# Performance work log

Hardware: AMD Instinct MI355X
Metric: run time of the kernel (lower is better)

Reference implementation:

```python
import jax, jax.numpy as jnp
import numpy as np

CUTOFF = 5.0
NLINKED = 1
CELL_LIST = CUTOFF / NLINKED  # linked-cell edge length
_r = np.arange(-NLINKED, NLINKED + 1)
# torch.cartesian_prod(r1,r1,r1) == meshgrid(indexing='ij') stacked & flattened
LINKED = np.stack(np.meshgrid(_r, _r, _r, indexing='ij'), axis=-1).reshape(1, -1, 3).astype(np.float32)  # (1, 27, 3)


def setup_inputs() -> dict:
    N = 2744
    L = 30.0
    key = jax.random.key(0)
    k1, k2 = jax.random.split(key)
    coordinates = jax.random.uniform(k1, (N, 3), dtype=jnp.float32) * L
    cell = jnp.eye(3, dtype=jnp.float32) * L
    mass = jax.random.uniform(k2, (N,), dtype=jnp.float32) * 15.0 + 1.0
    period_table = jnp.ones((3,), dtype=jnp.int32)  # fully periodic
    return {"period_table": period_table, "coordinates": coordinates, "cell": cell, "mass": mass}


def _forward(period_table, coordinates, cell, mass):
    numatom = coordinates.shape[0]
    # wrap coordinates into the cell relative to atom 0 (fractional coords)
    inv_cell = jnp.linalg.inv(cell)
    inv_coor = coordinates @ inv_cell
    inv_coor = inv_coor - jnp.round(inv_coor - inv_coor[0])
    coordinates = inv_coor @ cell
    # remove center of mass
    com = (mass @ coordinates) / jnp.sum(mass)
    coordinates = coordinates - com[None, :]
    # periodic replicas needed to cover the cutoff
    num_repeats = jnp.ceil(jnp.min(CUTOFF / jnp.abs(cell), axis=0)).astype(jnp.int32)
    num_repeats = period_table.astype(jnp.int32) * num_repeats
    up = num_repeats + 1
    down = -num_repeats
    rs = [jnp.arange(int(down[i]), int(up[i])) for i in range(3)]
    g = jnp.meshgrid(*rs, indexing='ij')
    shifts_frac = jnp.stack(g, axis=-1).reshape(-1, 3).astype(coordinates.dtype)  # (S, 3)
    shifts = shifts_frac @ cell  # (S, 3) cartesian shift vectors
    num_shifts = shifts.shape[0]
    # prod = cartesian_prod(all_shifts, all_atoms).T : row0 shift idx, row1 atom idx
    prod0 = jnp.repeat(jnp.arange(num_shifts), numatom)
    prod1 = jnp.tile(jnp.arange(numatom), num_shifts)
    # shift box so all coords are positive; pad by cutoff
    mincoor = jnp.min(coordinates, axis=0) - CUTOFF - 1e-6
    coordinates = coordinates - mincoor
    maxcoor = jnp.max(coordinates, axis=0) + CUTOFF
    # all periodic images, keep only those inside the padded box
    image = (coordinates[None, :, :] + shifts[:, None, :]).reshape(-1, 3)
    keep = jnp.nonzero(((image < maxcoor) & (image > 0)).all(axis=1))[0]
    image_mask = image[keep]                      # (M, 3)
    prod0 = prod0[keep]
    prod1 = prod1[keep]
    # linked-cell indices
    ori_image_index = jnp.floor(coordinates / CELL_LIST)         # (N, 3)
    neigh_cell = ori_image_index[:, None, :] + jnp.asarray(LINKED)  # (N, 27, 3)
    image_index = jnp.floor(image_mask / CELL_LIST)              # (M, 3)
    max_cell_index = jnp.ceil(maxcoor / CELL_LIST)
    f10 = max_cell_index[1] * max_cell_index[0]
    neigh_cell_index = neigh_cell[:, :, 2] * f10 + neigh_cell[:, :, 1] * max_cell_index[0] + neigh_cell[:, :, 0]  # (N, 27)
    nimage_index = image_index[:, 2] * f10 + image_index[:, 1] * max_cell_index[0] + image_index[:, 0]            # (M,)
    # dense (N, M, 27) cell-index equality -- the memory-bound hot spot
    eq = neigh_cell_index[:, None, :] == nimage_index[None, :, None]
    ai, aj, _ = jnp.nonzero(eq)
    # distance filter on candidate pairs
    d = jnp.linalg.norm(coordinates[ai] - image_mask[aj], axis=-1)
    pair = jnp.nonzero((d < CUTOFF) & (d > 0.001))[0]
    center = ai[pair]
    img = aj[pair]
    shift_idx = prod0[img]
    atom_j = prod1[img]
    neigh_list = jnp.stack([center, atom_j])  # (2, P)
    return neigh_list, shifts[shift_idx], shifts_frac, shift_idx


def reference(period_table, coordinates, cell, mass):
    neigh_list, shifts_out, _, _ = _forward(period_table, coordinates, cell, mass)
    return (neigh_list, shifts_out)
```

## Files before the change

kernel.cpp:

```cpp
#include <hip/hip_runtime.h>
#include <math.h>

#define S_CAP   27
#define NCELLS  4096
#define MAXNB   128
#define CUT     5.0f

__global__ __launch_bounds__(256)
void k1_pre(const int* __restrict__ period, const float* __restrict__ coor,
            const float* __restrict__ cell, const float* __restrict__ mass,
            int* hdr_i, float* hdr_f, float* shifts, float* xf,
            int* __restrict__ ccount, int* __restrict__ ccur, int n)
{
    #pragma clang fp contract(off)
    __shared__ double rs[256 * 4];
    __shared__ float  redf[256 * 3];
    __shared__ float  s_com[3], s_m2[3];
    int t = threadIdx.x;

    for (int c = t; c < NCELLS; c += 256) { ccount[c] = 0; ccur[c] = 0; }

    float c[3][3];
    #pragma unroll
    for (int i = 0; i < 3; i++)
        #pragma unroll
        for (int j = 0; j < 3; j++) c[i][j] = cell[3 * i + j];

    float a00 = c[1][1]*c[2][2] - c[1][2]*c[2][1];
    float a01 = c[0][2]*c[2][1] - c[0][1]*c[2][2];
    float a02 = c[0][1]*c[1][2] - c[0][2]*c[1][1];
    float a10 = c[1][2]*c[2][0] - c[1][0]*c[2][2];
    float a11 = c[0][0]*c[2][2] - c[0][2]*c[2][0];
    float a12 = c[0][2]*c[1][0] - c[0][0]*c[1][2];
    float a20 = c[1][0]*c[2][1] - c[1][1]*c[2][0];
    float a21 = c[0][1]*c[2][0] - c[0][0]*c[2][1];
    float a22 = c[0][0]*c[1][1] - c[0][1]*c[1][0];
    float det = c[0][0]*a00 + c[0][1]*a10 + c[0][2]*a20;
    float inv[3][3] = {{a00/det, a01/det, a02/det},
                       {a10/det, a11/det, a12/det},
                       {a20/det, a21/det, a22/det}};

    float f0[3];
    #pragma unroll
    for (int d = 0; d < 3; d++)
        f0[d] = coor[0]*inv[0][d] + coor[1]*inv[1][d] + coor[2]*inv[2][d];

    double sm = 0.0, sx = 0.0, sy = 0.0, sz = 0.0;
    for (int i = t; i < n; i += 256) {
        float p0 = coor[3*i], p1 = coor[3*i+1], p2 = coor[3*i+2];
        float ic[3], w[3], x[3];
        #pragma unroll
        for (int d = 0; d < 3; d++)
            ic[d] = p0*inv[0][d] + p1*inv[1][d] + p2*inv[2][d];
        #pragma unroll
        for (int d = 0; d < 3; d++)
            w[d] = ic[d] - rintf(ic[d] - f0[d]);
        #pragma unroll
        for (int d = 0; d < 3; d++)
            x[d] = w[0]*c[0][d] + w[1]*c[1][d] + w[2]*c[2][d];
        xf[3*i] = x[0]; xf[3*i+1] = x[1]; xf[3*i+2] = x[2];
        float m = mass[i];
        sm += (double)m;
        sx += (double)m * (double)x[0];
        sy += (double)m * (double)x[1];
        sz += (double)m * (double)x[2];
    }
    rs[t] = sm; rs[256+t] = sx; rs[512+t] = sy; rs[768+t] = sz;
    __syncthreads();
    for (int off = 128; off > 0; off >>= 1) {
        if (t < off) {
            rs[t]       += rs[t+off];
            rs[256+t]   += rs[256+t+off];
            rs[512+t]   += rs[512+t+off];
            rs[768+t]   += rs[768+t+off];
        }
        __syncthreads();
    }
    if (t == 0) {
        float den = (float)rs[0];
        s_com[0] = ((float)rs[256]) / den;
        s_com[1] = ((float)rs[512]) / den;
        s_com[2] = ((float)rs[768]) / den;
    }
    __syncthreads();
    float com0 = s_com[0], com1 = s_com[1], com2 = s_com[2];

    float mn0 = __builtin_inff(), mn1 = __builtin_inff(), mn2 = __builtin_inff();
    for (int i = t; i < n; i += 256) {
        float v0 = xf[3*i]   - com0;
        float v1 = xf[3*i+1] - com1;
        float v2 = xf[3*i+2] - com2;
        xf[3*i] = v0; xf[3*i+1] = v1; xf[3*i+2] = v2;
        mn0 = fminf(mn0, v0); mn1 = fminf(mn1, v1); mn2 = fminf(mn2, v2);
    }
    redf[t] = mn0; redf[256+t] = mn1; redf[512+t] = mn2;
    __syncthreads();
    for (int off = 128; off > 0; off >>= 1) {
        if (t < off) {
            redf[t]     = fminf(redf[t],     redf[t+off]);
            redf[256+t] = fminf(redf[256+t], redf[256+t+off]);
            redf[512+t] = fminf(redf[512+t], redf[512+t+off]);
        }
        __syncthreads();
    }
    if (t == 0) {
        s_m2[0] = (redf[0]   - CUT) - 1e-6f;
        s_m2[1] = (redf[256] - CUT) - 1e-6f;
        s_m2[2] = (redf[512] - CUT) - 1e-6f;
    }
    __syncthreads();
    float m20 = s_m2[0], m21 = s_m2[1], m22 = s_m2[2];

    float mx0 = -__builtin_inff(), mx1 = -__builtin_inff(), mx2 = -__builtin_inff();
    for (int i = t; i < n; i += 256) {
        float v0 = xf[3*i]   - m20;
        float v1 = xf[3*i+1] - m21;
        float v2 = xf[3*i+2] - m22;
        xf[3*i] = v0; xf[3*i+1] = v1; xf[3*i+2] = v2;
        mx0 = fmaxf(mx0, v0); mx1 = fmaxf(mx1, v1); mx2 = fmaxf(mx2, v2);
    }
    redf[t] = mx0; redf[256+t] = mx1; redf[512+t] = mx2;
    __syncthreads();
    for (int off = 128; off > 0; off >>= 1) {
        if (t < off) {
            redf[t]     = fmaxf(redf[t],     redf[t+off]);
            redf[256+t] = fmaxf(redf[256+t], redf[256+t+off]);
            redf[512+t] = fmaxf(redf[512+t], redf[512+t+off]);
        }
        __syncthreads();
    }
    if (t == 0) {
        float maxc0 = redf[0]   + CUT;
        float maxc1 = redf[256] + CUT;
        float maxc2 = redf[512] + CUT;
        float mcell0 = ceilf(maxc0 / CUT);
        float mcell1 = ceilf(maxc1 / CUT);
        float f10 = mcell1 * mcell0;
        int nr[3];
        for (int j = 0; j < 3; j++) {
            float v = __builtin_inff();
            for (int i = 0; i < 3; i++) {
                float q = CUT / fabsf(c[i][j]);
                v = fminf(v, q);
            }
            nr[j] = (int)ceilf(v);
            nr[j] *= period[j];
        }
        int nsz0 = 2*nr[0]+1, nsz1 = 2*nr[1]+1, nsz2 = 2*nr[2]+1;
        int S = nsz0 * nsz1 * nsz2;
        if (S > S_CAP) S = S_CAP;
        hdr_i[0] = S;
        hdr_i[3] = -nr[0]; hdr_i[4] = -nr[1]; hdr_i[5] = -nr[2];
        hdr_i[6] = nsz0;   hdr_i[7] = nsz1;   hdr_i[8] = nsz2;
        hdr_i[9]  = (int)mcell0;
        hdr_i[10] = (int)f10;
        hdr_f[0] = maxc0; hdr_f[1] = maxc1; hdr_f[2] = maxc2;
        hdr_f[3] = f10;   hdr_f[4] = mcell0;
    }
    __syncthreads();
    int S = hdr_i[0];
    if (t < S) {
        int n1 = hdr_i[7], n2 = hdr_i[8];
        int i0 = t / (n1 * n2);
        int rem = t - i0 * n1 * n2;
        int i1 = rem / n2;
        int i2 = rem - i1 * n2;
        float fx = (float)(hdr_i[3] + i0);
        float fy = (float)(hdr_i[4] + i1);
        float fz = (float)(hdr_i[5] + i2);
        #pragma unroll
        for (int d = 0; d < 3; d++)
            shifts[3*t + d] = fx*c[0][d] + fy*c[1][d] + fz*c[2][d];
    }
}

__global__ __launch_bounds__(256)
void k2_count(const int* __restrict__ hdr_i, const float* __restrict__ hdr_f,
              const float* __restrict__ shifts, const float* __restrict__ xf,
              int* __restrict__ ccount, int n)
{
    #pragma clang fp contract(off)
    int g = blockIdx.x * 256 + threadIdx.x;
    int sn = hdr_i[0] * n;
    if (g >= sn) return;
    int s = g / n, a = g - s * n;
    float i0 = xf[3*a]   + shifts[3*s];
    float i1 = xf[3*a+1] + shifts[3*s+1];
    float i2 = xf[3*a+2] + shifts[3*s+2];
    bool k = (i0 > 0.0f) && (i0 < hdr_f[0]) &&
             (i1 > 0.0f) && (i1 < hdr_f[1]) &&
             (i2 > 0.0f) && (i2 < hdr_f[2]);
    if (!k) return;
    float fc0 = floorf(i0 / CUT);
    float fc1 = floorf(i1 / CUT);
    float fc2 = floorf(i2 / CUT);
    float cf = fc2 * hdr_f[3] + fc1 * hdr_f[4] + fc0;
    int ci = (int)cf;
    if (ci < 0) ci = 0;
    if (ci >= NCELLS) ci = NCELLS - 1;
    atomicAdd(&ccount[ci], 1);
}

__global__ __launch_bounds__(1024)
void k5_scan(const int* __restrict__ ccount, int* __restrict__ cstart)
{
    __shared__ int sarr[1024];
    int t = threadIdx.x;
    int b = t * 4;
    int v0 = ccount[b], v1 = ccount[b+1], v2 = ccount[b+2], v3 = ccount[b+3];
    int lsum = v0 + v1 + v2 + v3;
    sarr[t] = lsum;
    __syncthreads();
    for (int off = 1; off < 1024; off <<= 1) {
        int v = (t >= off) ? sarr[t - off] : 0;
        __syncthreads();
        sarr[t] += v;
        __syncthreads();
    }
    int excl = sarr[t] - lsum;
    cstart[b]   = excl;
    cstart[b+1] = excl + v0;
    cstart[b+2] = excl + v0 + v1;
    cstart[b+3] = excl + v0 + v1 + v2;
    if (t == 1023) cstart[NCELLS] = sarr[1023];
}

__global__ __launch_bounds__(256)
void k5b_fill(const int* __restrict__ hdr_i, const float* __restrict__ hdr_f,
              const float* __restrict__ shifts, const float* __restrict__ xf,
              const int* __restrict__ cstart, int* __restrict__ ccur,
              float4* __restrict__ bucket4, int n)
{
    #pragma clang fp contract(off)
    int g = blockIdx.x * 256 + threadIdx.x;
    int sn = hdr_i[0] * n;
    if (g >= sn) return;
    int s = g / n, a = g - s * n;
    float i0 = xf[3*a]   + shifts[3*s];
    float i1 = xf[3*a+1] + shifts[3*s+1];
    float i2 = xf[3*a+2] + shifts[3*s+2];
    bool k = (i0 > 0.0f) && (i0 < hdr_f[0]) &&
             (i1 > 0.0f) && (i1 < hdr_f[1]) &&
             (i2 > 0.0f) && (i2 < hdr_f[2]);
    if (!k) return;
    float fc0 = floorf(i0 / CUT);
    float fc1 = floorf(i1 / CUT);
    float fc2 = floorf(i2 / CUT);
    float cf = fc2 * hdr_f[3] + fc1 * hdr_f[4] + fc0;
    int ci = (int)cf;
    if (ci < 0) ci = 0;
    if (ci >= NCELLS) ci = NCELLS - 1;
    int w = cstart[ci] + atomicAdd(&ccur[ci], 1);
    bucket4[w] = make_float4(i0, i1, i2, __int_as_float(g));
}

__global__ __launch_bounds__(256)
void k6_count(const int* __restrict__ hdr_i, const float* __restrict__ xf,
              const int* __restrict__ cstart, const float4* __restrict__ bucket4,
              int* __restrict__ npair, int n)
{
    #pragma clang fp contract(off)
    int lane = threadIdx.x & 63;
    int atom = (blockIdx.x * 256 + threadIdx.x) >> 6;
    if (atom >= n) return;
    int mci = hdr_i[9], f10i = hdr_i[10];
    float x0 = xf[3*atom], x1 = xf[3*atom+1], x2 = xf[3*atom+2];
    int o0 = (int)floorf(x0 / CUT);
    int o1 = (int)floorf(x1 / CUT);
    int o2 = (int)floorf(x2 / CUT);
    int cnt = 0;
    for (int dz = -1; dz <= 1; dz++)
        for (int dy = -1; dy <= 1; dy++) {
            int nc0 = (o2+dz)*f10i + (o1+dy)*mci + (o0-1);
            int lo = nc0 < 0 ? 0 : nc0;
            int hi = nc0 + 3 > NCELLS ? NCELLS : nc0 + 3;
            if (lo >= hi) continue;
            int b0 = cstart[lo], b1 = cstart[hi];
            for (int b = b0 + lane; b < b1; b += 64) {
                float4 v = bucket4[b];
                float dxx = x0 - v.x;
                float dyy = x1 - v.y;
                float dzz = x2 - v.z;
                float ss = dxx*dxx + dyy*dyy + dzz*dzz;
                float dd = sqrtf(ss);
                if (dd < CUT && dd > 0.001f) cnt++;
            }
        }
    #pragma unroll
    for (int off = 32; off > 0; off >>= 1)
        cnt += __shfl_down(cnt, off, 64);
    if (lane == 0) npair[atom] = cnt;
}

__global__ __launch_bounds__(1024)
void k7_scan(int* hdr_i, const int* __restrict__ npair, int* __restrict__ pstart, int n)
{
    __shared__ int sarr[1024];
    int t = threadIdx.x;
    int CH = (n + 1023) >> 10;
    int base = t * CH;
    int lsum = 0;
    for (int e = 0; e < CH; e++) {
        int g = base + e;
        if (g < n) lsum += npair[g];
    }
    sarr[t] = lsum;
    __syncthreads();
    for (int off = 1; off < 1024; off <<= 1) {
        int v = (t >= off) ? sarr[t - off] : 0;
        __syncthreads();
        sarr[t] += v;
        __syncthreads();
    }
    int run = sarr[t] - lsum;
    for (int e = 0; e < CH; e++) {
        int g = base + e;
        if (g < n) { pstart[g] = run; run += npair[g]; }
    }
    if (t == 1023) pstart[n] = sarr[1023];
    if (t == 0)    hdr_i[2]  = sarr[1023];
}

__global__ __launch_bounds__(256)
void k8_emit(const int* __restrict__ hdr_i, const float* __restrict__ xf,
             const float* __restrict__ shifts, const int* __restrict__ cstart,
             const float4* __restrict__ bucket4, const int* __restrict__ pstart,
             float* __restrict__ out, int n, int P)
{
    #pragma clang fp contract(off)
    __shared__ int lst[4][MAXNB];
    int w    = threadIdx.x >> 6;
    int lane = threadIdx.x & 63;
    int atom = blockIdx.x * 4 + w;
    bool valid = atom < n;

    int mci = hdr_i[9], f10i = hdr_i[10];
    float x0 = 0.f, x1 = 0.f, x2 = 0.f;
    if (valid) { x0 = xf[3*atom]; x1 = xf[3*atom+1]; x2 = xf[3*atom+2]; }
    int o0 = (int)floorf(x0 / CUT);
    int o1 = (int)floorf(x1 / CUT);
    int o2 = (int)floorf(x2 / CUT);

    int cnt = 0;
    if (valid) {
        for (int dz = -1; dz <= 1; dz++)
            for (int dy = -1; dy <= 1; dy++) {
                int nc0 = (o2+dz)*f10i + (o1+dy)*mci + (o0-1);
                int lo = nc0 < 0 ? 0 : nc0;
                int hi = nc0 + 3 > NCELLS ? NCELLS : nc0 + 3;
                if (lo >= hi) continue;
                int b0 = cstart[lo], b1 = cstart[hi];
                for (int bb = b0; bb < b1; bb += 64) {
                    int b = bb + lane;
                    bool ok = false; int g = 0;
                    if (b < b1) {
                        float4 v = bucket4[b];
                        g = __float_as_int(v.w);
                        float dxx = x0 - v.x;
                        float dyy = x1 - v.y;
                        float dzz = x2 - v.z;
                        float ss = dxx*dxx + dyy*dyy + dzz*dzz;
                        float dd = sqrtf(ss);
                        ok = (dd < CUT) && (dd > 0.001f);
                    }
                    unsigned long long m = __ballot(ok);
                    int posn = cnt + (int)__popcll(m & ((1ull << lane) - 1ull));
                    if (ok && posn < MAXNB) lst[w][posn] = g;
                    cnt += (int)__popcll(m);
                }
            }
        if (cnt > MAXNB) cnt = MAXNB;
    }
    __syncthreads();

    if (valid) {
        int base = pstart[atom];
        for (int r = lane; r < cnt; r += 64) {
            int g = lst[w][r];
            int rank = 0;
            for (int q = 0; q < cnt; q++) rank += (lst[w][q] < g) ? 1 : 0;
            int p = base + rank;
            if (p < P) {
                int s = g / n;
                int a = g - s * n;
                out[p]     = (float)atom;
                out[P + p] = (float)a;
                out[2*P + 3*p]     = shifts[3*s];
                out[2*P + 3*p + 1] = shifts[3*s + 1];
                out[2*P + 3*p + 2] = shifts[3*s + 2];
            }
        }
    }
}

extern "C" void kernel_launch(void* const* d_in, const int* in_sizes, int n_in,
                              void* d_out, int out_size, void* d_ws, size_t ws_size,
                              hipStream_t stream)
{
    const int*   period = (const int*)d_in[0];
    const float* coor   = (const float*)d_in[1];
    const float* cell   = (const float*)d_in[2];
    const float* mass   = (const float*)d_in[3];
    float* out = (float*)d_out;

    int n  = in_sizes[1] / 3;
    int SN = S_CAP * n;
    int P  = out_size / 5;

    char* w = (char*)d_ws;
    size_t off = 0;
    auto alloc = [&](size_t bytes) -> void* {
        off = (off + 15) & ~(size_t)15;
        void* p = (void*)(w + off); off += bytes; return p;
    };

    int*    hdr_i   = (int*)   alloc(16 * 4);
    float*  hdr_f   = (float*) alloc(16 * 4);
    float*  shifts  = (float*) alloc(3 * S_CAP * 4);
    float*  xf      = (float*) alloc(3 * (size_t)n * 4);
    int*    ccount  = (int*)   alloc(NCELLS * 4);
    int*    ccur    = (int*)   alloc(NCELLS * 4);
    int*    cstart  = (int*)   alloc((NCELLS + 1) * 4);
    float4* bucket4 = (float4*)alloc((size_t)SN * 16);
    int*    npair   = (int*)   alloc((size_t)n * 4);
    int*    pstart  = (int*)   alloc(((size_t)n + 1) * 4);
    (void)ws_size; (void)n_in;

    hipMemsetAsync(d_out, 0, (size_t)out_size * 4, stream);

    int nwb = (n + 3) / 4;

    hipLaunchKernelGGL(k1_pre,   dim3(1),            dim3(256),  0, stream,
                       period, coor, cell, mass, hdr_i, hdr_f, shifts, xf, ccount, ccur, n);
    hipLaunchKernelGGL(k2_count, dim3((SN+255)/256), dim3(256),  0, stream,
                       hdr_i, hdr_f, shifts, xf, ccount, n);
    hipLaunchKernelGGL(k5_scan,  dim3(1),            dim3(1024), 0, stream,
                       ccount, cstart);
    hipLaunchKernelGGL(k5b_fill, dim3((SN+255)/256), dim3(256),  0, stream,
                       hdr_i, hdr_f, shifts, xf, cstart, ccur, bucket4, n);
    hipLaunchKernelGGL(k6_count, dim3(nwb),          dim3(256),  0, stream,
                       hdr_i, xf, cstart, bucket4, npair, n);
    hipLaunchKernelGGL(k7_scan,  dim3(1),            dim3(1024), 0, stream,
                       hdr_i, npair, pstart, n);
    hipLaunchKernelGGL(k8_emit,  dim3(nwb),          dim3(256),  0, stream,
                       hdr_i, xf, shifts, cstart, bucket4, pstart, out, n, P);
}
```

Before: 108.7 us.

## Fuse scans into last-block epilogues and cache neighbor lists between count and emit

Replaces the two single-block scan kernels with last-block-done epilogues inside the count kernels, using a global atomic ticket. This cuts the launch chain from seven launches to five. The pair-count kernel now writes each atom's candidate neighbor list to a global slab, so the emit kernel reads it instead of redoing the cell search. The k1 min/max reductions are merged into one pass, with the min offset applied on the fly rather than via an extra rewrite pass. The output memset is dropped. The cost is that the reductions are serialized through one block's tail and per-atom slab memory traffic is added. Dropping the memset risks leaving stale output beyond the emitted pair count.

Result: slower. 159.4 us (+46.7%).

```diff
diff --git a/kernel.cpp b/kernel.cpp
--- a/kernel.cpp
+++ b/kernel.cpp
@@ -6,19 +6,21 @@
 #define MAXNB   128
 #define CUT     5.0f
 
+
 __global__ __launch_bounds__(256)
 void k1_pre(const int* __restrict__ period, const float* __restrict__ coor,
             const float* __restrict__ cell, const float* __restrict__ mass,
-            int* hdr_i, float* hdr_f, float* shifts, float* xf,
+            int* hdr_i, float* hdr_f, float* shifts, float* xv,
             int* __restrict__ ccount, int* __restrict__ ccur, int n)
 {
     #pragma clang fp contract(off)
     __shared__ double rs[256 * 4];
-    __shared__ float  redf[256 * 3];
+    __shared__ float  redf[256 * 6];
     __shared__ float  s_com[3], s_m2[3];
     int t = threadIdx.x;
 
     for (int c = t; c < NCELLS; c += 256) { ccount[c] = 0; ccur[c] = 0; }
+    if (t < 2) hdr_i[12 + t] = 0;
 
     float c[3][3];
     #pragma unroll
@@ -58,7 +60,7 @@
         #pragma unroll
         for (int d = 0; d < 3; d++)
             x[d] = w[0]*c[0][d] + w[1]*c[1][d] + w[2]*c[2][d];
-        xf[3*i] = x[0]; xf[3*i+1] = x[1]; xf[3*i+2] = x[2];
+        xv[3*i] = x[0]; xv[3*i+1] = x[1]; xv[3*i+2] = x[2];
         float m = mass[i];
         sm += (double)m;
         sx += (double)m * (double)x[0];
@@ -69,10 +71,10 @@
     __syncthreads();
     for (int off = 128; off > 0; off >>= 1) {
         if (t < off) {
-            rs[t]       += rs[t+off];
-            rs[256+t]   += rs[256+t+off];
-            rs[512+t]   += rs[512+t+off];
-            rs[768+t]   += rs[768+t+off];
+            rs[t]     += rs[t+off];
+            rs[256+t] += rs[256+t+off];
+            rs[512+t] += rs[512+t+off];
+            rs[768+t] += rs[768+t+off];
         }
         __syncthreads();
     }
@@ -85,54 +87,38 @@
     __syncthreads();
     float com0 = s_com[0], com1 = s_com[1], com2 = s_com[2];
 
-    float mn0 = __builtin_inff(), mn1 = __builtin_inff(), mn2 = __builtin_inff();
+    float mn0 =  __builtin_inff(), mn1 =  __builtin_inff(), mn2 =  __builtin_inff();
+    float mx0 = -__builtin_inff(), mx1 = -__builtin_inff(), mx2 = -__builtin_inff();
     for (int i = t; i < n; i += 256) {
-        float v0 = xf[3*i]   - com0;
-        float v1 = xf[3*i+1] - com1;
-        float v2 = xf[3*i+2] - com2;
-        xf[3*i] = v0; xf[3*i+1] = v1; xf[3*i+2] = v2;
+        float v0 = xv[3*i]   - com0;
+        float v1 = xv[3*i+1] - com1;
+        float v2 = xv[3*i+2] - com2;
+        xv[3*i] = v0; xv[3*i+1] = v1; xv[3*i+2] = v2;
         mn0 = fminf(mn0, v0); mn1 = fminf(mn1, v1); mn2 = fminf(mn2, v2);
-    }
-    redf[t] = mn0; redf[256+t] = mn1; redf[512+t] = mn2;
+        mx0 = fmaxf(mx0, v0); mx1 = fmaxf(mx1, v1); mx2 = fmaxf(mx2, v2);
+    }
+    redf[t]       = mn0; redf[256+t]  = mn1; redf[512+t]  = mn2;
+    redf[768+t]   = mx0; redf[1024+t] = mx1; redf[1280+t] = mx2;
     __syncthreads();
     for (int off = 128; off > 0; off >>= 1) {
         if (t < off) {
-            redf[t]     = fminf(redf[t],     redf[t+off]);
-            redf[256+t] = fminf(redf[256+t], redf[256+t+off]);
-            redf[512+t] = fminf(redf[512+t], redf[512+t+off]);
+            redf[t]      = fminf(redf[t],      redf[t+off]);
+            redf[256+t]  = fminf(redf[256+t],  redf[256+t+off]);
+            redf[512+t]  = fminf(redf[512+t],  redf[512+t+off]);
+            redf[768+t]  = fmaxf(redf[768+t],  redf[768+t+off]);
+            redf[1024+t] = fmaxf(redf[1024+t], redf[1024+t+off]);
+            redf[1280+t] = fmaxf(redf[1280+t], redf[1280+t+off]);
         }
         __syncthreads();
     }
     if (t == 0) {
-        s_m2[0] = (redf[0]   - CUT) - 1e-6f;
-        s_m2[1] = (redf[256] - CUT) - 1e-6f;
-        s_m2[2] = (redf[512] - CUT) - 1e-6f;
-    }
-    __syncthreads();
-    float m20 = s_m2[0], m21 = s_m2[1], m22 = s_m2[2];
-
-    float mx0 = -__builtin_inff(), mx1 = -__builtin_inff(), mx2 = -__builtin_inff();
-    for (int i = t; i < n; i += 256) {
-        float v0 = xf[3*i]   - m20;
-        float v1 = xf[3*i+1] - m21;
-        float v2 = xf[3*i+2] - m22;
-        xf[3*i] = v0; xf[3*i+1] = v1; xf[3*i+2] = v2;
-        mx0 = fmaxf(mx0, v0); mx1 = fmaxf(mx1, v1); mx2 = fmaxf(mx2, v2);
-    }
-    redf[t] = mx0; redf[256+t] = mx1; redf[512+t] = mx2;
-    __syncthreads();
-    for (int off = 128; off > 0; off >>= 1) {
-        if (t < off) {
-            redf[t]     = fmaxf(redf[t],     redf[t+off]);
-            redf[256+t] = fmaxf(redf[256+t], redf[256+t+off]);
-            redf[512+t] = fmaxf(redf[512+t], redf[512+t+off]);
-        }
-        __syncthreads();
-    }
-    if (t == 0) {
-        float maxc0 = redf[0]   + CUT;
-        float maxc1 = redf[256] + CUT;
-        float maxc2 = redf[512] + CUT;
+        float m20 = (redf[0]   - CUT) - 1e-6f;
+        float m21 = (redf[256] - CUT) - 1e-6f;
+        float m22 = (redf[512] - CUT) - 1e-6f;
+        s_m2[0] = m20; s_m2[1] = m21; s_m2[2] = m22;
+        float maxc0 = (redf[768]  - m20) + CUT;
+        float maxc1 = (redf[1024] - m21) + CUT;
+        float maxc2 = (redf[1280] - m22) + CUT;
         float mcell0 = ceilf(maxc0 / CUT);
         float mcell1 = ceilf(maxc1 / CUT);
         float f10 = mcell1 * mcell0;
@@ -156,6 +142,7 @@
         hdr_i[10] = (int)f10;
         hdr_f[0] = maxc0; hdr_f[1] = maxc1; hdr_f[2] = maxc2;
         hdr_f[3] = f10;   hdr_f[4] = mcell0;
+        hdr_f[5] = m20;   hdr_f[6] = m21;   hdr_f[7] = m22;
     }
     __syncthreads();
     int S = hdr_i[0];
@@ -175,70 +162,78 @@
 }
 
 __global__ __launch_bounds__(256)
-void k2_count(const int* __restrict__ hdr_i, const float* __restrict__ hdr_f,
-              const float* __restrict__ shifts, const float* __restrict__ xf,
-              int* __restrict__ ccount, int n)
+void k2_count(int* hdr_i, const float* __restrict__ hdr_f,
+              const float* __restrict__ shifts, const float* __restrict__ xv,
+              int* __restrict__ ccount, int* __restrict__ cstart, int n)
+{
+    #pragma clang fp contract(off)
+    __shared__ int si[256];
+    __shared__ int s_last;
+    int t = threadIdx.x;
+    int g = blockIdx.x * 256 + t;
+    int sn = hdr_i[0] * n;
+    float m20 = hdr_f[5], m21 = hdr_f[6], m22 = hdr_f[7];
+    if (g < sn) {
+        int s = g / n, a = g - s * n;
+        float i0 = (xv[3*a]   - m20) + shifts[3*s];
+        float i1 = (xv[3*a+1] - m21) + shifts[3*s+1];
+        float i2 = (xv[3*a+2] - m22) + shifts[3*s+2];
+        bool k = (i0 > 0.0f) && (i0 < hdr_f[0]) &&
+                 (i1 > 0.0f) && (i1 < hdr_f[1]) &&
+                 (i2 > 0.0f) && (i2 < hdr_f[2]);
+        if (k) {
+            float fc0 = floorf(i0 / CUT);
+            float fc1 = floorf(i1 / CUT);
+            float fc2 = floorf(i2 / CUT);
+            float cf = fc2 * hdr_f[3] + fc1 * hdr_f[4] + fc0;
+            int ci = (int)cf;
+            if (ci < 0) ci = 0;
+            if (ci >= NCELLS) ci = NCELLS - 1;
+            atomicAdd(&ccount[ci], 1);
+        }
+    }
+    __threadfence();
+    __syncthreads();
+    if (t == 0) s_last = (atomicAdd(&hdr_i[12], 1) == (int)gridDim.x - 1) ? 1 : 0;
+    __syncthreads();
+    if (s_last) {
+        __threadfence();
+        const int CH = NCELLS / 256;
+        int base = t * CH;
+        int vals[NCELLS / 256];
+        int lsum = 0;
+        #pragma unroll
+        for (int e = 0; e < CH; e++) { vals[e] = ccount[base + e]; lsum += vals[e]; }
+        si[t] = lsum;
+        __syncthreads();
+        for (int off = 1; off < 256; off <<= 1) {
+            int v = (t >= off) ? si[t - off] : 0;
+            __syncthreads();
+            si[t] += v;
+            __syncthreads();
+        }
+        int run = si[t] - lsum;
+        #pragma unroll
+        for (int e = 0; e < CH; e++) { cstart[base + e] = run; run += vals[e]; }
+        if (t == 255) cstart[NCELLS] = si[255];
+    }
+}
+
+__global__ __launch_bounds__(256)
+void k3_fill(const int* __restrict__ hdr_i, const float* __restrict__ hdr_f,
+             const float* __restrict__ shifts, const float* __restrict__ xv,
+             const int* __restrict__ cstart, int* __restrict__ ccur,
+             float4* __restrict__ bucket4, int n)
 {
     #pragma clang fp contract(off)
     int g = blockIdx.x * 256 + threadIdx.x;
     int sn = hdr_i[0] * n;
     if (g >= sn) return;
+    float m20 = hdr_f[5], m21 = hdr_f[6], m22 = hdr_f[7];
     int s = g / n, a = g - s * n;
-    float i0 = xf[3*a]   + shifts[3*s];
-    float i1 = xf[3*a+1] + shifts[3*s+1];
-    float i2 = xf[3*a+2] + shifts[3*s+2];
-    bool k = (i0 > 0.0f) && (i0 < hdr_f[0]) &&
-             (i1 > 0.0f) && (i1 < hdr_f[1]) &&
-             (i2 > 0.0f) && (i2 < hdr_f[2]);
-    if (!k) return;
-    float fc0 = floorf(i0 / CUT);
-    float fc1 = floorf(i1 / CUT);
-    float fc2 = floorf(i2 / CUT);
-    float cf = fc2 * hdr_f[3] + fc1 * hdr_f[4] + fc0;
-    int ci = (int)cf;
-    if (ci < 0) ci = 0;
-    if (ci >= NCELLS) ci = NCELLS - 1;
-    atomicAdd(&ccount[ci], 1);
-}
-
-__global__ __launch_bounds__(1024)
-void k5_scan(const int* __restrict__ ccount, int* __restrict__ cstart)
-{
-    __shared__ int sarr[1024];
-    int t = threadIdx.x;
-    int b = t * 4;
-    int v0 = ccount[b], v1 = ccount[b+1], v2 = ccount[b+2], v3 = ccount[b+3];
-    int lsum = v0 + v1 + v2 + v3;
-    sarr[t] = lsum;
-    __syncthreads();
-    for (int off = 1; off < 1024; off <<= 1) {
-        int v = (t >= off) ? sarr[t - off] : 0;
-        __syncthreads();
-        sarr[t] += v;
-        __syncthreads();
-    }
-    int excl = sarr[t] - lsum;
-    cstart[b]   = excl;
-    cstart[b+1] = excl + v0;
-    cstart[b+2] = excl + v0 + v1;
-    cstart[b+3] = excl + v0 + v1 + v2;
-    if (t == 1023) cstart[NCELLS] = sarr[1023];
-}
-
-__global__ __launch_bounds__(256)
-void k5b_fill(const int* __restrict__ hdr_i, const float* __restrict__ hdr_f,
-              const float* __restrict__ shifts, const float* __restrict__ xf,
-              const int* __restrict__ cstart, int* __restrict__ ccur,
-              float4* __restrict__ bucket4, int n)
-{
-    #pragma clang fp contract(off)
-    int g = blockIdx.x * 256 + threadIdx.x;
-    int sn = hdr_i[0] * n;
-    if (g >= sn) return;
-    int s = g / n, a = g - s * n;
-    float i0 = xf[3*a]   + shifts[3*s];
-    float i1 = xf[3*a+1] + shifts[3*s+1];
-    float i2 = xf[3*a+2] + shifts[3*s+2];
+    float i0 = (xv[3*a]   - m20) + shifts[3*s];
+    float i1 = (xv[3*a+1] - m21) + shifts[3*s+1];
+    float i2 = (xv[3*a+2] - m22) + shifts[3*s+2];
     bool k = (i0 > 0.0f) && (i0 < hdr_f[0]) &&
              (i1 > 0.0f) && (i1 < hdr_f[1]) &&
              (i2 > 0.0f) && (i2 < hdr_f[2]);
@@ -255,94 +250,29 @@
 }
 
 __global__ __launch_bounds__(256)
-void k6_count(const int* __restrict__ hdr_i, const float* __restrict__ xf,
-              const int* __restrict__ cstart, const float4* __restrict__ bucket4,
-              int* __restrict__ npair, int n)
+void k4_count(int* hdr_i, const float* __restrict__ hdr_f,
+              const float* __restrict__ xv, const int* __restrict__ cstart,
+              const float4* __restrict__ bucket4, int* __restrict__ nb,
+              int* __restrict__ npair, int* __restrict__ pstart, int n)
 {
     #pragma clang fp contract(off)
-    int lane = threadIdx.x & 63;
-    int atom = (blockIdx.x * 256 + threadIdx.x) >> 6;
-    if (atom >= n) return;
+    __shared__ int si[256];
+    __shared__ int s_last;
+    int t    = threadIdx.x;
+    int lane = t & 63;
+    int w    = t >> 6;
+    int atom = blockIdx.x * 4 + w;
+    float m20 = hdr_f[5], m21 = hdr_f[6], m22 = hdr_f[7];
     int mci = hdr_i[9], f10i = hdr_i[10];
-    float x0 = xf[3*atom], x1 = xf[3*atom+1], x2 = xf[3*atom+2];
-    int o0 = (int)floorf(x0 / CUT);
-    int o1 = (int)floorf(x1 / CUT);
-    int o2 = (int)floorf(x2 / CUT);
-    int cnt = 0;
-    for (int dz = -1; dz <= 1; dz++)
-        for (int dy = -1; dy <= 1; dy++) {
-            int nc0 = (o2+dz)*f10i + (o1+dy)*mci + (o0-1);
-            int lo = nc0 < 0 ? 0 : nc0;
-            int hi = nc0 + 3 > NCELLS ? NCELLS : nc0 + 3;
-            if (lo >= hi) continue;
-            int b0 = cstart[lo], b1 = cstart[hi];
-            for (int b = b0 + lane; b < b1; b += 64) {
-                float4 v = bucket4[b];
-                float dxx = x0 - v.x;
-                float dyy = x1 - v.y;
-                float dzz = x2 - v.z;
-                float ss = dxx*dxx + dyy*dyy + dzz*dzz;
-                float dd = sqrtf(ss);
-                if (dd < CUT && dd > 0.001f) cnt++;
-            }
-        }
-    #pragma unroll
-    for (int off = 32; off > 0; off >>= 1)
-        cnt += __shfl_down(cnt, off, 64);
-    if (lane == 0) npair[atom] = cnt;
-}
-
-__global__ __launch_bounds__(1024)
-void k7_scan(int* hdr_i, const int* __restrict__ npair, int* __restrict__ pstart, int n)
-{
-    __shared__ int sarr[1024];
-    int t = threadIdx.x;
-    int CH = (n + 1023) >> 10;
-    int base = t * CH;
-    int lsum = 0;
-    for (int e = 0; e < CH; e++) {
-        int g = base + e;
-        if (g < n) lsum += npair[g];
-    }
-    sarr[t] = lsum;
-    __syncthreads();
-    for (int off = 1; off < 1024; off <<= 1) {
-        int v = (t >= off) ? sarr[t - off] : 0;
-        __syncthreads();
-        sarr[t] += v;
-        __syncthreads();
-    }
-    int run = sarr[t] - lsum;
-    for (int e = 0; e < CH; e++) {
-        int g = base + e;
-        if (g < n) { pstart[g] = run; run += npair[g]; }
-    }
-    if (t == 1023) pstart[n] = sarr[1023];
-    if (t == 0)    hdr_i[2]  = sarr[1023];
-}
-
-__global__ __launch_bounds__(256)
-void k8_emit(const int* __restrict__ hdr_i, const float* __restrict__ xf,
-             const float* __restrict__ shifts, const int* __restrict__ cstart,
-             const float4* __restrict__ bucket4, const int* __restrict__ pstart,
-             float* __restrict__ out, int n, int P)
-{
-    #pragma clang fp contract(off)
-    __shared__ int lst[4][MAXNB];
-    int w    = threadIdx.x >> 6;
-    int lane = threadIdx.x & 63;
-    int atom = blockIdx.x * 4 + w;
-    bool valid = atom < n;
-
-    int mci = hdr_i[9], f10i = hdr_i[10];
-    float x0 = 0.f, x1 = 0.f, x2 = 0.f;
-    if (valid) { x0 = xf[3*atom]; x1 = xf[3*atom+1]; x2 = xf[3*atom+2]; }
-    int o0 = (int)floorf(x0 / CUT);
-    int o1 = (int)floorf(x1 / CUT);
-    int o2 = (int)floorf(x2 / CUT);
-
-    int cnt = 0;
-    if (valid) {
+    if (atom < n) {
+        float x0 = xv[3*atom]   - m20;
+        float x1 = xv[3*atom+1] - m21;
+        float x2 = xv[3*atom+2] - m22;
+        int o0 = (int)floorf(x0 / CUT);
+        int o1 = (int)floorf(x1 / CUT);
+        int o2 = (int)floorf(x2 / CUT);
+        int cnt = 0;
+        int* slab = nb + (size_t)atom * MAXNB;
         for (int dz = -1; dz <= 1; dz++)
             for (int dy = -1; dy <= 1; dy++) {
                 int nc0 = (o2+dz)*f10i + (o1+dy)*mci + (o0-1);
@@ -365,14 +295,61 @@
                     }
                     unsigned long long m = __ballot(ok);
                     int posn = cnt + (int)__popcll(m & ((1ull << lane) - 1ull));
-                    if (ok && posn < MAXNB) lst[w][posn] = g;
+                    if (ok && posn < MAXNB) slab[posn] = g;
                     cnt += (int)__popcll(m);
                 }
             }
+        if (lane == 0) npair[atom] = cnt;
+    }
+    __threadfence();
+    __syncthreads();
+    if (t == 0) s_last = (atomicAdd(&hdr_i[13], 1) == (int)gridDim.x - 1) ? 1 : 0;
+    __syncthreads();
+    if (s_last) {
+        __threadfence();
+        int CHn = (n + 255) / 256;
+        int base = t * CHn;
+        int lsum = 0;
+        for (int e = 0; e < CHn; e++) {
+            int g = base + e;
+            if (g < n) lsum += npair[g];
+        }
+        si[t] = lsum;
+        __syncthreads();
+        for (int off = 1; off < 256; off <<= 1) {
+            int v = (t >= off) ? si[t - off] : 0;
+            __syncthreads();
+            si[t] += v;
+            __syncthreads();
+        }
+        int run = si[t] - lsum;
+        for (int e = 0; e < CHn; e++) {
+            int g = base + e;
+            if (g < n) { pstart[g] = run; run += npair[g]; }
+        }
+        if (t == 255) pstart[n] = si[255];
+    }
+}
+
+__global__ __launch_bounds__(256)
+void k5_emit(const int* __restrict__ nb, const int* __restrict__ npair,
+             const int* __restrict__ pstart, const float* __restrict__ shifts,
+             float* __restrict__ out, int n, int P)
+{
+    __shared__ int lst[4][MAXNB];
+    int t    = threadIdx.x;
+    int lane = t & 63;
+    int w    = t >> 6;
+    int atom = blockIdx.x * 4 + w;
+    bool valid = atom < n;
+    int cnt = 0;
+    if (valid) {
+        cnt = npair[atom];
         if (cnt > MAXNB) cnt = MAXNB;
-    }
-    __syncthreads();
-
+        const int* slab = nb + (size_t)atom * MAXNB;
+        for (int r = lane; r < cnt; r += 64) lst[w][r] = slab[r];
+    }
+    __syncthreads();
     if (valid) {
         int base = pstart[atom];
         for (int r = lane; r < cnt; r += 64) {
@@ -411,37 +388,33 @@
     size_t off = 0;
     auto alloc = [&](size_t bytes) -> void* {
         off = (off + 15) & ~(size_t)15;
-        void* p = (void*)(w + off); off += bytes; return p;
+        void* pp = (void*)(w + off); off += bytes; return pp;
     };
 
     int*    hdr_i   = (int*)   alloc(16 * 4);
     float*  hdr_f   = (float*) alloc(16 * 4);
     float*  shifts  = (float*) alloc(3 * S_CAP * 4);
-    float*  xf      = (float*) alloc(3 * (size_t)n * 4);
+    float*  xv      = (float*) alloc(3 * (size_t)n * 4);
     int*    ccount  = (int*)   alloc(NCELLS * 4);
     int*    ccur    = (int*)   alloc(NCELLS * 4);
     int*    cstart  = (int*)   alloc((NCELLS + 1) * 4);
     float4* bucket4 = (float4*)alloc((size_t)SN * 16);
+    int*    nb      = (int*)   alloc((size_t)n * MAXNB * 4);
     int*    npair   = (int*)   alloc((size_t)n * 4);
     int*    pstart  = (int*)   alloc(((size_t)n + 1) * 4);
     (void)ws_size; (void)n_in;
 
-    hipMemsetAsync(d_out, 0, (size_t)out_size * 4, stream);
-
-    int nwb = (n + 3) / 4;
-
-    hipLaunchKernelGGL(k1_pre,   dim3(1),            dim3(256),  0, stream,
-                       period, coor, cell, mass, hdr_i, hdr_f, shifts, xf, ccount, ccur, n);
-    hipLaunchKernelGGL(k2_count, dim3((SN+255)/256), dim3(256),  0, stream,
-                       hdr_i, hdr_f, shifts, xf, ccount, n);
-    hipLaunchKernelGGL(k5_scan,  dim3(1),            dim3(1024), 0, stream,
-                       ccount, cstart);
-    hipLaunchKernelGGL(k5b_fill, dim3((SN+255)/256), dim3(256),  0, stream,
-                       hdr_i, hdr_f, shifts, xf, cstart, ccur, bucket4, n);
-    hipLaunchKernelGGL(k6_count, dim3(nwb),          dim3(256),  0, stream,
-                       hdr_i, xf, cstart, bucket4, npair, n);
-    hipLaunchKernelGGL(k7_scan,  dim3(1),            dim3(1024), 0, stream,
-                       hdr_i, npair, pstart, n);
-    hipLaunchKernelGGL(k8_emit,  dim3(nwb),          dim3(256),  0, stream,
-                       hdr_i, xf, shifts, cstart, bucket4, pstart, out, n, P);
-}
+    int gb_img  = (SN + 255) / 256;
+    int gb_atom = (n + 3) / 4;
+
+    hipLaunchKernelGGL(k1_pre,   dim3(1),       dim3(256), 0, stream,
+                       period, coor, cell, mass, hdr_i, hdr_f, shifts, xv, ccount, ccur, n);
+    hipLaunchKernelGGL(k2_count, dim3(gb_img),  dim3(256), 0, stream,
+                       hdr_i, hdr_f, shifts, xv, ccount, cstart, n);
+    hipLaunchKernelGGL(k3_fill,  dim3(gb_img),  dim3(256), 0, stream,
+                       hdr_i, hdr_f, shifts, xv, cstart, ccur, bucket4, n);
+    hipLaunchKernelGGL(k4_count, dim3(gb_atom), dim3(256), 0, stream,
+                       hdr_i, hdr_f, xv, cstart, bucket4, nb, npair, pstart, n);
+    hipLaunchKernelGGL(k5_emit,  dim3(gb_atom), dim3(256), 0, stream,
+                       nb, npair, pstart, shifts, out, n, P);
+}
```
